# Kernel optimization log

Measured on AMD Instinct MI355X. Metric: run time of the kernel, lower is better.

## Reference

```python
import jax, jax.numpy as jnp
import numpy as np


def setup_inputs() -> dict:
    key = jax.random.key(0)
    kx, kw = jax.random.split(key)
    x = jax.random.normal(kx, (32, 256, 56, 56), dtype=jnp.float32)
    weight = jax.random.uniform(kw, (256, 256, 3, 3), dtype=jnp.float32) * 0.001
    return {"x": x, "weight": weight}


def reference(x, weight):
    # --- binarize activations with straight-through estimator ---
    # forward value = sign(x); gradient flows through clamp(x, -1, 1)
    clipped_x = jnp.clip(x, -1.0, 1.0)
    bx = jax.lax.stop_gradient(jnp.sign(x) - clipped_x) + clipped_x

    # --- binarize weights (per-output-channel mean-centered, scaled sign) ---
    w = weight
    # subtract per-output-channel mean over (in_c, kh, kw)
    bw = w - jnp.mean(w.reshape(w.shape[0], -1), axis=-1)[:, None, None, None]
    # per-output-channel scaling factor = mean |bw| (detached)
    scale = jnp.mean(jnp.abs(bw), axis=(1, 2, 3), keepdims=True)
    scale = jax.lax.stop_gradient(scale)
    clipped_w = jnp.clip(bw, -1.0, 1.0)
    binary_w = jax.lax.stop_gradient(scale * jnp.sign(bw) - clipped_w) + clipped_w

    # --- conv2d, NCHW / OIHW, stride 1, padding 1 ---
    y = jax.lax.conv_general_dilated(
        bx, binary_w,
        window_strides=(1, 1),
        padding=((1, 1), (1, 1)),
        dimension_numbers=("NCHW", "OIHW", "NCHW"),
    )
    return y
```

## Files before the change

kernel.cpp:

```cpp
#include <hip/hip_runtime.h>
#include <cstdint>
#include <cstddef>

#define N_ 32
#define C_ 256
#define H_ 56
#define W_ 56

typedef int v4i __attribute__((ext_vector_type(4)));

static constexpr size_t WB_BYTES = 36ull * 16 * 64 * 16;
static constexpr size_t SC_OFF   = WB_BYTES;

__device__ __forceinline__ uint32_t sgnw(uint32_t u) {
    return (u & 0x7fffffffu) ? (((uint32_t)(((int)u) >> 31) | 1u) & 0xffu) : 0u;
}

__global__ __launch_bounds__(256) void pack_w(const float* __restrict__ wt,
                                              char* __restrict__ wB,
                                              float* __restrict__ scaleg) {
    __shared__ double red[256];
    int o = blockIdx.x, tid = threadIdx.x;
    const float* wo = wt + (size_t)o * 2304;

    double s = 0;
    for (int j = tid; j < 2304; j += 256) s += (double)wo[j];
    red[tid] = s;
    __syncthreads();
    for (int k = 128; k > 0; k >>= 1) {
        if (tid < k) red[tid] += red[tid + k];
        __syncthreads();
    }
    double mean = red[0] / 2304.0;
    __syncthreads();

    double s2 = 0;
    for (int j = tid; j < 2304; j += 256) s2 += fabs((double)wo[j] - mean);
    red[tid] = s2;
    __syncthreads();
    for (int k = 128; k > 0; k >>= 1) {
        if (tid < k) red[tid] += red[tid + k];
        __syncthreads();
    }
    if (tid == 0) scaleg[o] = (float)(red[0] / 2304.0);

    if (tid < 144) {
        int kiter = tid >> 2, q = tid & 3;
        int tap = kiter >> 2, cb = kiter & 3;
        int kh = tap / 3, kw = tap - kh * 3;
        int words[4];
        for (int g = 0; g < 4; ++g) {
            int word = 0;
            for (int b = 0; b < 4; ++b) {
                int c = cb * 64 + q * 16 + g * 4 + b;
                double v = (double)wo[c * 9 + kh * 3 + kw];
                int sg = (v > mean) - (v < mean);
                word |= (sg & 0xff) << (8 * b);
            }
            words[g] = word;
        }
        v4i pk = {words[0], words[1], words[2], words[3]};
        *(v4i*)(wB + (((size_t)kiter * 16 + (o >> 4)) * 64 + q * 16 + (o & 15)) * 16) = pk;
    }
}

__global__ __launch_bounds__(512, 2) void conv_mfma(const float* __restrict__ x,
                                                    const v4i* __restrict__ wB,
                                                    const float* __restrict__ scaleg,
                                                    float* __restrict__ out) {
    __shared__ char xs[6 * 58 * 256];
    int tid = threadIdx.x;
    int wave = tid >> 6, lane = tid & 63;
    int hq = blockIdx.x, n = blockIdx.y;
    int h0 = hq * 4;

    if (tid < 192) {
        int r  = tid >> 5;
        int c2 = tid & 31;
        int wp = (c2 >> 4) * 57;
        int ch = c2 & 15;
        int slot = (ch + wp) & 15;
        v4i z = {0, 0, 0, 0};
        *(v4i*)(xs + ((size_t)(r * 58 + wp) << 8) + (slot << 4)) = z;
    }
    for (int u = tid; u < 6 * 16 * 14; u += 512) {
        int R   = u / 224;
        int rem = u - R * 224;
        int ch  = rem / 14;
        int wq  = rem - ch * 14;
        int ir  = h0 + R - 1;
        if (ir < 0 || ir > 55) {
            v4i z = {0, 0, 0, 0};
#pragma unroll
            for (int h = 0; h < 4; ++h) {
                int wp = 1 + wq * 4 + h;
                int slot = (ch + wp) & 15;
                *(v4i*)(xs + ((size_t)(R * 58 + wp) << 8) + (slot << 4)) = z;
            }
            continue;
        }
        const float* xb = x + ((size_t)n * C_ + ch * 16) * 3136 + ir * 56 + wq * 4;
        uint32_t t[4][4];
#pragma unroll
        for (int p = 0; p < 4; ++p) {
            uint32_t w0, w1, w2, w3;
            {
                float4 v = *(const float4*)(xb + (size_t)(4 * p + 0) * 3136);
                w0 = sgnw(__float_as_uint(v.x)) | (sgnw(__float_as_uint(v.y)) << 8) |
                     (sgnw(__float_as_uint(v.z)) << 16) | (sgnw(__float_as_uint(v.w)) << 24);
            }
            {
                float4 v = *(const float4*)(xb + (size_t)(4 * p + 1) * 3136);
                w1 = sgnw(__float_as_uint(v.x)) | (sgnw(__float_as_uint(v.y)) << 8) |
                     (sgnw(__float_as_uint(v.z)) << 16) | (sgnw(__float_as_uint(v.w)) << 24);
            }
            {
                float4 v = *(const float4*)(xb + (size_t)(4 * p + 2) * 3136);
                w2 = sgnw(__float_as_uint(v.x)) | (sgnw(__float_as_uint(v.y)) << 8) |
                     (sgnw(__float_as_uint(v.z)) << 16) | (sgnw(__float_as_uint(v.w)) << 24);
            }
            {
                float4 v = *(const float4*)(xb + (size_t)(4 * p + 3) * 3136);
                w3 = sgnw(__float_as_uint(v.x)) | (sgnw(__float_as_uint(v.y)) << 8) |
                     (sgnw(__float_as_uint(v.z)) << 16) | (sgnw(__float_as_uint(v.w)) << 24);
            }
            uint32_t lo01 = __builtin_amdgcn_perm(w1, w0, 0x05010400u);
            uint32_t hi01 = __builtin_amdgcn_perm(w1, w0, 0x07030602u);
            uint32_t lo23 = __builtin_amdgcn_perm(w3, w2, 0x05010400u);
            uint32_t hi23 = __builtin_amdgcn_perm(w3, w2, 0x07030602u);
            t[p][0] = __builtin_amdgcn_perm(lo23, lo01, 0x05040100u);
            t[p][1] = __builtin_amdgcn_perm(lo23, lo01, 0x07060302u);
            t[p][2] = __builtin_amdgcn_perm(hi23, hi01, 0x05040100u);
            t[p][3] = __builtin_amdgcn_perm(hi23, hi01, 0x07060302u);
        }
#pragma unroll
        for (int h = 0; h < 4; ++h) {
            int wp = 1 + wq * 4 + h;
            int slot = (ch + wp) & 15;
            v4i c4 = {(int)t[0][h], (int)t[1][h], (int)t[2][h], (int)t[3][h]};
            *(v4i*)(xs + ((size_t)(R * 58 + wp) << 8) + (slot << 4)) = c4;
        }
    }

    int lm = lane & 15, q = lane >> 4;
    int og = wave & 3, mg = wave >> 2;
    int kstart = __builtin_amdgcn_readfirstlane((9 * wave) >> 1);

    int posb[7], slotb[7];
#pragma unroll
    for (int mf = 0; mf < 7; ++mf) {
        int m = mg * 112 + mf * 16 + lm;
        int r = m / 56;
        int wof = m - r * 56;
        posb[mf]  = r * 58 + wof;
        slotb[mf] = q + wof;
    }

    v4i acc[7][4];
#pragma unroll
    for (int mf = 0; mf < 7; ++mf)
#pragma unroll
        for (int of = 0; of < 4; ++of) { v4i z = {0, 0, 0, 0}; acc[mf][of] = z; }

    const v4i* wBw = wB + (size_t)(og * 4) * 64 + lane;

    auto wrap = [&](int t) { int k = kstart + t; return k >= 36 ? k - 36 : k; };
    auto loadB = [&](int k, v4i (&b)[4]) {
#pragma unroll
        for (int of = 0; of < 4; ++of) b[of] = wBw[(size_t)k * 1024 + of * 64];
    };

    __syncthreads();

    v4i bR0[4], bR1[4], bR2[4];
    loadB(wrap(0), bR0);
    loadB(wrap(1), bR1);
    loadB(wrap(2), bR2);

    auto step = [&](v4i (&bReg)[4], int t) {
        int k = wrap(t);
        int tap = k >> 2, cb = k & 3;
        int dh = (tap * 11) >> 5;
        int dw = tap - dh * 3;
        int pofs = dh * 58 + dw;
        int sofs = cb * 4 + dw;
        v4i a[7];
#pragma unroll
        for (int mf = 0; mf < 7; ++mf) {
            int pos  = posb[mf] + pofs;
            int slot = (slotb[mf] + sofs) & 15;
            a[mf] = *(const v4i*)(xs + ((size_t)pos << 8) + ((size_t)slot << 4));
        }
        __builtin_amdgcn_s_setprio(1);
#pragma unroll
        for (int mf = 0; mf < 7; ++mf)
#pragma unroll
            for (int of = 0; of < 4; ++of)
                acc[mf][of] = __builtin_amdgcn_mfma_i32_16x16x64_i8(
                    a[mf], bReg[of], acc[mf][of], 0, 0, 0);
        __builtin_amdgcn_s_setprio(0);
        loadB(wrap(t + 3), bReg);
    };

    for (int t3 = 0; t3 < 12; ++t3) {
        int t = t3 * 3;
        step(bR0, t);
        step(bR1, t + 1);
        step(bR2, t + 2);
    }

#pragma unroll
    for (int of = 0; of < 4; ++of) {
        int o = og * 64 + of * 16 + lm;
        float s = scaleg[o];
#pragma unroll
        for (int mf = 0; mf < 7; ++mf) {
            int m  = mg * 112 + mf * 16 + q * 4;
            int r  = m / 56;
            int wb = m - r * 56;
            float* ob = out + ((size_t)(n * C_ + o) * H_ + h0 + r) * W_ + wb;
            float4 v = {s * (float)acc[mf][of].x, s * (float)acc[mf][of].y,
                        s * (float)acc[mf][of].z, s * (float)acc[mf][of].w};
            *(float4*)ob = v;
        }
    }
}

extern "C" void kernel_launch(void* const* d_in, const int* in_sizes, int n_in,
                              void* d_out, int out_size, void* d_ws, size_t ws_size,
                              hipStream_t stream) {
    const float* x   = (const float*)d_in[0];
    const float* wgt = (const float*)d_in[1];
    float* out = (float*)d_out;
    char* ws = (char*)d_ws;

    char*  wb = ws;
    float* sg = (float*)(ws + SC_OFF);

    pack_w<<<dim3(256), dim3(256), 0, stream>>>(wgt, wb, sg);
    conv_mfma<<<dim3(14, N_), dim3(512), 0, stream>>>(x, (const v4i*)wb, sg, out);
}
```

Before: 246.9 us.

## Overlap halo-row staging with first MFMA steps and swizzle block order

The kernel now stages only the first four input rows into LDS before compute. The last two rows are loaded and packed by half the threads during the first twelve k-steps, which only use taps dh=0,1, and then a barrier precedes the remaining steps. The per-wave k order is reworked so every wave starts within the first 12 k-indices, and block IDs are swizzled to group batches for cache locality. Launch bounds drop to one block per CU, which gives more registers to the prefetch buffers but may reduce latency hiding from occupancy.

```diff
diff --git a/kernel.cpp b/kernel.cpp
--- a/kernel.cpp
+++ b/kernel.cpp
@@ -14,6 +14,10 @@
 
 __device__ __forceinline__ uint32_t sgnw(uint32_t u) {
     return (u & 0x7fffffffu) ? (((uint32_t)(((int)u) >> 31) | 1u) & 0xffu) : 0u;
+}
+__device__ __forceinline__ uint32_t pack4(float4 v) {
+    return sgnw(__float_as_uint(v.x)) | (sgnw(__float_as_uint(v.y)) << 8) |
+           (sgnw(__float_as_uint(v.z)) << 16) | (sgnw(__float_as_uint(v.w)) << 24);
 }
 
 __global__ __launch_bounds__(256) void pack_w(const float* __restrict__ wt,
@@ -64,14 +68,17 @@
     }
 }
 
-__global__ __launch_bounds__(512, 2) void conv_mfma(const float* __restrict__ x,
+__global__ __launch_bounds__(512, 1) void conv_mfma(const float* __restrict__ x,
                                                     const v4i* __restrict__ wB,
                                                     const float* __restrict__ scaleg,
                                                     float* __restrict__ out) {
     __shared__ char xs[6 * 58 * 256];
     int tid = threadIdx.x;
     int wave = tid >> 6, lane = tid & 63;
-    int hq = blockIdx.x, n = blockIdx.y;
+
+    int lin = blockIdx.x + 14 * blockIdx.y;
+    int swz = (lin & 7) * 56 + (lin >> 3);
+    int hq = swz % 14, n = swz / 14;
     int h0 = hq * 4;
 
     if (tid < 192) {
@@ -83,13 +90,13 @@
         v4i z = {0, 0, 0, 0};
         *(v4i*)(xs + ((size_t)(r * 58 + wp) << 8) + (slot << 4)) = z;
     }
-    for (int u = tid; u < 6 * 16 * 14; u += 512) {
+    for (int u = tid; u < 896; u += 512) {
         int R   = u / 224;
         int rem = u - R * 224;
         int ch  = rem / 14;
         int wq  = rem - ch * 14;
         int ir  = h0 + R - 1;
-        if (ir < 0 || ir > 55) {
+        if (ir < 0) {
             v4i z = {0, 0, 0, 0};
 #pragma unroll
             for (int h = 0; h < 4; ++h) {
@@ -100,34 +107,17 @@
             continue;
         }
         const float* xb = x + ((size_t)n * C_ + ch * 16) * 3136 + ir * 56 + wq * 4;
+        uint32_t sw[16];
+#pragma unroll
+        for (int c = 0; c < 16; ++c)
+            sw[c] = pack4(*(const float4*)(xb + (size_t)c * 3136));
         uint32_t t[4][4];
 #pragma unroll
         for (int p = 0; p < 4; ++p) {
-            uint32_t w0, w1, w2, w3;
-            {
-                float4 v = *(const float4*)(xb + (size_t)(4 * p + 0) * 3136);
-                w0 = sgnw(__float_as_uint(v.x)) | (sgnw(__float_as_uint(v.y)) << 8) |
-                     (sgnw(__float_as_uint(v.z)) << 16) | (sgnw(__float_as_uint(v.w)) << 24);
-            }
-            {
-                float4 v = *(const float4*)(xb + (size_t)(4 * p + 1) * 3136);
-                w1 = sgnw(__float_as_uint(v.x)) | (sgnw(__float_as_uint(v.y)) << 8) |
-                     (sgnw(__float_as_uint(v.z)) << 16) | (sgnw(__float_as_uint(v.w)) << 24);
-            }
-            {
-                float4 v = *(const float4*)(xb + (size_t)(4 * p + 2) * 3136);
-                w2 = sgnw(__float_as_uint(v.x)) | (sgnw(__float_as_uint(v.y)) << 8) |
-                     (sgnw(__float_as_uint(v.z)) << 16) | (sgnw(__float_as_uint(v.w)) << 24);
-            }
-            {
-                float4 v = *(const float4*)(xb + (size_t)(4 * p + 3) * 3136);
-                w3 = sgnw(__float_as_uint(v.x)) | (sgnw(__float_as_uint(v.y)) << 8) |
-                     (sgnw(__float_as_uint(v.z)) << 16) | (sgnw(__float_as_uint(v.w)) << 24);
-            }
-            uint32_t lo01 = __builtin_amdgcn_perm(w1, w0, 0x05010400u);
-            uint32_t hi01 = __builtin_amdgcn_perm(w1, w0, 0x07030602u);
-            uint32_t lo23 = __builtin_amdgcn_perm(w3, w2, 0x05010400u);
-            uint32_t hi23 = __builtin_amdgcn_perm(w3, w2, 0x07030602u);
+            uint32_t lo01 = __builtin_amdgcn_perm(sw[4*p+1], sw[4*p+0], 0x05010400u);
+            uint32_t hi01 = __builtin_amdgcn_perm(sw[4*p+1], sw[4*p+0], 0x07030602u);
+            uint32_t lo23 = __builtin_amdgcn_perm(sw[4*p+3], sw[4*p+2], 0x05010400u);
+            uint32_t hi23 = __builtin_amdgcn_perm(sw[4*p+3], sw[4*p+2], 0x07030602u);
             t[p][0] = __builtin_amdgcn_perm(lo23, lo01, 0x05040100u);
             t[p][1] = __builtin_amdgcn_perm(lo23, lo01, 0x07060302u);
             t[p][2] = __builtin_amdgcn_perm(hi23, hi01, 0x05040100u);
@@ -142,9 +132,34 @@
         }
     }
 
+    bool su = (tid < 448);
+    int sR = 0, sch = 0, swq = 0;
+    bool sload = false;
+    const float* sxb = nullptr;
+    if (su) {
+        sR  = 4 + (tid / 224);
+        int rem = tid - (sR - 4) * 224;
+        sch = rem / 14;
+        swq = rem - sch * 14;
+        int sir = h0 + sR - 1;
+        sload = (sir <= 55);
+        if (sload)
+            sxb = x + ((size_t)n * C_ + sch * 16) * 3136 + sir * 56 + swq * 4;
+        else {
+            v4i z = {0, 0, 0, 0};
+#pragma unroll
+            for (int h = 0; h < 4; ++h) {
+                int wp = 1 + swq * 4 + h;
+                int slot = (sch + wp) & 15;
+                *(v4i*)(xs + ((size_t)(sR * 58 + wp) << 8) + (slot << 4)) = z;
+            }
+        }
+    }
+
+    __syncthreads();
+
     int lm = lane & 15, q = lane >> 4;
     int og = wave & 3, mg = wave >> 2;
-    int kstart = __builtin_amdgcn_readfirstlane((9 * wave) >> 1);
 
     int posb[7], slotb[7];
 #pragma unroll
@@ -164,21 +179,28 @@
 
     const v4i* wBw = wB + (size_t)(og * 4) * 64 + lane;
 
-    auto wrap = [&](int t) { int k = kstart + t; return k >= 36 ? k - 36 : k; };
+    auto kof = [&](int t) {
+        if (t >= 36) t -= 36;
+        return (t < 12) ? ((wave + t) % 12) : (12 + (3 * wave + (t - 12)) % 24);
+    };
     auto loadB = [&](int k, v4i (&b)[4]) {
 #pragma unroll
         for (int of = 0; of < 4; ++of) b[of] = wBw[(size_t)k * 1024 + of * 64];
     };
 
-    __syncthreads();
+    float4 fa[8];
+    if (su && sload) {
+#pragma unroll
+        for (int c = 0; c < 8; ++c) fa[c] = *(const float4*)(sxb + (size_t)c * 3136);
+    }
 
     v4i bR0[4], bR1[4], bR2[4];
-    loadB(wrap(0), bR0);
-    loadB(wrap(1), bR1);
-    loadB(wrap(2), bR2);
+    loadB(kof(0), bR0);
+    loadB(kof(1), bR1);
+    loadB(kof(2), bR2);
 
     auto step = [&](v4i (&bReg)[4], int t) {
-        int k = wrap(t);
+        int k = kof(t);
         int tap = k >> 2, cb = k & 3;
         int dh = (tap * 11) >> 5;
         int dw = tap - dh * 3;
@@ -199,14 +221,50 @@
                 acc[mf][of] = __builtin_amdgcn_mfma_i32_16x16x64_i8(
                     a[mf], bReg[of], acc[mf][of], 0, 0, 0);
         __builtin_amdgcn_s_setprio(0);
-        loadB(wrap(t + 3), bReg);
+        loadB(kof(t + 3), bReg);
     };
 
-    for (int t3 = 0; t3 < 12; ++t3) {
-        int t = t3 * 3;
-        step(bR0, t);
-        step(bR1, t + 1);
-        step(bR2, t + 2);
+    uint32_t sw_[16];
+    step(bR0, 0);  step(bR1, 1);  step(bR2, 2);
+    step(bR0, 3);  step(bR1, 4);  step(bR2, 5);
+    if (su && sload) {
+#pragma unroll
+        for (int c = 0; c < 8; ++c) sw_[c] = pack4(fa[c]);
+#pragma unroll
+        for (int c = 0; c < 8; ++c) fa[c] = *(const float4*)(sxb + (size_t)(8 + c) * 3136);
+    }
+    step(bR0, 6);  step(bR1, 7);  step(bR2, 8);
+    step(bR0, 9);  step(bR1, 10); step(bR2, 11);
+    if (su && sload) {
+#pragma unroll
+        for (int c = 0; c < 8; ++c) sw_[8 + c] = pack4(fa[c]);
+        uint32_t t[4][4];
+#pragma unroll
+        for (int p = 0; p < 4; ++p) {
+            uint32_t lo01 = __builtin_amdgcn_perm(sw_[4*p+1], sw_[4*p+0], 0x05010400u);
+            uint32_t hi01 = __builtin_amdgcn_perm(sw_[4*p+1], sw_[4*p+0], 0x07030602u);
+            uint32_t lo23 = __builtin_amdgcn_perm(sw_[4*p+3], sw_[4*p+2], 0x05010400u);
+            uint32_t hi23 = __builtin_amdgcn_perm(sw_[4*p+3], sw_[4*p+2], 0x07030602u);
+            t[p][0] = __builtin_amdgcn_perm(lo23, lo01, 0x05040100u);
+            t[p][1] = __builtin_amdgcn_perm(lo23, lo01, 0x07060302u);
+            t[p][2] = __builtin_amdgcn_perm(hi23, hi01, 0x05040100u);
+            t[p][3] = __builtin_amdgcn_perm(hi23, hi01, 0x07060302u);
+        }
+#pragma unroll
+        for (int h = 0; h < 4; ++h) {
+            int wp = 1 + swq * 4 + h;
+            int slot = (sch + wp) & 15;
+            v4i c4 = {(int)t[0][h], (int)t[1][h], (int)t[2][h], (int)t[3][h]};
+            *(v4i*)(xs + ((size_t)(sR * 58 + wp) << 8) + (slot << 4)) = c4;
+        }
+    }
+    asm volatile("s_waitcnt lgkmcnt(0)" ::: "memory");
+    __builtin_amdgcn_s_barrier();
+    __builtin_amdgcn_sched_barrier(0);
+#pragma unroll 2
+    for (int g = 0; g < 8; ++g) {
+        int t = 12 + 3 * g;
+        step(bR0, t); step(bR1, t + 1); step(bR2, t + 2);
     }
 
 #pragma unroll
```

Measured after the change: 384.4 us. 1.56x slower.

## Shrink conv tile to two output rows with 4 waves and swizzled block order

Applied to the files above, without the earlier changes.

Each block now computes two output rows instead of four, using 256 threads (4 waves, each owning 64 output channels) and a 4-row LDS halo tile. This gives twice as many blocks to spread across CUs and uses less LDS per block. A block-index swizzle interleaves images across consecutive blocks, and the activation sign-packing now issues all 16 channel loads before the byte permutes. In exchange, the halo overhead grows (4 input rows per 2 output rows instead of 6 per 4), and each weight fragment is reused across fewer output rows.

```diff
diff --git a/kernel.cpp b/kernel.cpp
--- a/kernel.cpp
+++ b/kernel.cpp
@@ -14,6 +14,10 @@
 
 __device__ __forceinline__ uint32_t sgnw(uint32_t u) {
     return (u & 0x7fffffffu) ? (((uint32_t)(((int)u) >> 31) | 1u) & 0xffu) : 0u;
+}
+__device__ __forceinline__ uint32_t pack4(float4 v) {
+    return sgnw(__float_as_uint(v.x)) | (sgnw(__float_as_uint(v.y)) << 8) |
+           (sgnw(__float_as_uint(v.z)) << 16) | (sgnw(__float_as_uint(v.w)) << 24);
 }
 
 __global__ __launch_bounds__(256) void pack_w(const float* __restrict__ wt,
@@ -64,17 +68,20 @@
     }
 }
 
-__global__ __launch_bounds__(512, 2) void conv_mfma(const float* __restrict__ x,
+__global__ __launch_bounds__(256, 2) void conv_mfma(const float* __restrict__ x,
                                                     const v4i* __restrict__ wB,
                                                     const float* __restrict__ scaleg,
                                                     float* __restrict__ out) {
-    __shared__ char xs[6 * 58 * 256];
+    __shared__ char xs[4 * 58 * 256];
     int tid = threadIdx.x;
     int wave = tid >> 6, lane = tid & 63;
-    int hq = blockIdx.x, n = blockIdx.y;
-    int h0 = hq * 4;
-
-    if (tid < 192) {
+
+    int lin = blockIdx.x + 28 * blockIdx.y;
+    int swz = (lin & 7) * 112 + (lin >> 3);
+    int hp = swz % 28, n = swz / 28;
+    int h0 = hp * 2;
+
+    if (tid < 128) {
         int r  = tid >> 5;
         int c2 = tid & 31;
         int wp = (c2 >> 4) * 57;
@@ -83,7 +90,7 @@
         v4i z = {0, 0, 0, 0};
         *(v4i*)(xs + ((size_t)(r * 58 + wp) << 8) + (slot << 4)) = z;
     }
-    for (int u = tid; u < 6 * 16 * 14; u += 512) {
+    for (int u = tid; u < 896; u += 256) {
         int R   = u / 224;
         int rem = u - R * 224;
         int ch  = rem / 14;
@@ -100,34 +107,17 @@
             continue;
         }
         const float* xb = x + ((size_t)n * C_ + ch * 16) * 3136 + ir * 56 + wq * 4;
+        uint32_t sw[16];
+#pragma unroll
+        for (int c = 0; c < 16; ++c)
+            sw[c] = pack4(*(const float4*)(xb + (size_t)c * 3136));
         uint32_t t[4][4];
 #pragma unroll
         for (int p = 0; p < 4; ++p) {
-            uint32_t w0, w1, w2, w3;
-            {
-                float4 v = *(const float4*)(xb + (size_t)(4 * p + 0) * 3136);
-                w0 = sgnw(__float_as_uint(v.x)) | (sgnw(__float_as_uint(v.y)) << 8) |
-                     (sgnw(__float_as_uint(v.z)) << 16) | (sgnw(__float_as_uint(v.w)) << 24);
-            }
-            {
-                float4 v = *(const float4*)(xb + (size_t)(4 * p + 1) * 3136);
-                w1 = sgnw(__float_as_uint(v.x)) | (sgnw(__float_as_uint(v.y)) << 8) |
-                     (sgnw(__float_as_uint(v.z)) << 16) | (sgnw(__float_as_uint(v.w)) << 24);
-            }
-            {
-                float4 v = *(const float4*)(xb + (size_t)(4 * p + 2) * 3136);
-                w2 = sgnw(__float_as_uint(v.x)) | (sgnw(__float_as_uint(v.y)) << 8) |
-                     (sgnw(__float_as_uint(v.z)) << 16) | (sgnw(__float_as_uint(v.w)) << 24);
-            }
-            {
-                float4 v = *(const float4*)(xb + (size_t)(4 * p + 3) * 3136);
-                w3 = sgnw(__float_as_uint(v.x)) | (sgnw(__float_as_uint(v.y)) << 8) |
-                     (sgnw(__float_as_uint(v.z)) << 16) | (sgnw(__float_as_uint(v.w)) << 24);
-            }
-            uint32_t lo01 = __builtin_amdgcn_perm(w1, w0, 0x05010400u);
-            uint32_t hi01 = __builtin_amdgcn_perm(w1, w0, 0x07030602u);
-            uint32_t lo23 = __builtin_amdgcn_perm(w3, w2, 0x05010400u);
-            uint32_t hi23 = __builtin_amdgcn_perm(w3, w2, 0x07030602u);
+            uint32_t lo01 = __builtin_amdgcn_perm(sw[4*p+1], sw[4*p+0], 0x05010400u);
+            uint32_t hi01 = __builtin_amdgcn_perm(sw[4*p+1], sw[4*p+0], 0x07030602u);
+            uint32_t lo23 = __builtin_amdgcn_perm(sw[4*p+3], sw[4*p+2], 0x05010400u);
+            uint32_t hi23 = __builtin_amdgcn_perm(sw[4*p+3], sw[4*p+2], 0x07030602u);
             t[p][0] = __builtin_amdgcn_perm(lo23, lo01, 0x05040100u);
             t[p][1] = __builtin_amdgcn_perm(lo23, lo01, 0x07060302u);
             t[p][2] = __builtin_amdgcn_perm(hi23, hi01, 0x05040100u);
@@ -143,13 +133,13 @@
     }
 
     int lm = lane & 15, q = lane >> 4;
-    int og = wave & 3, mg = wave >> 2;
-    int kstart = __builtin_amdgcn_readfirstlane((9 * wave) >> 1);
+    int og = wave;
+    int kstart = __builtin_amdgcn_readfirstlane(wave * 9);
 
     int posb[7], slotb[7];
 #pragma unroll
     for (int mf = 0; mf < 7; ++mf) {
-        int m = mg * 112 + mf * 16 + lm;
+        int m = mf * 16 + lm;
         int r = m / 56;
         int wof = m - r * 56;
         posb[mf]  = r * 58 + wof;
@@ -164,7 +154,12 @@
 
     const v4i* wBw = wB + (size_t)(og * 4) * 64 + lane;
 
-    auto wrap = [&](int t) { int k = kstart + t; return k >= 36 ? k - 36 : k; };
+    auto wrap = [&](int t) {
+        int k = kstart + t;
+        if (k >= 36) k -= 36;
+        if (k >= 36) k -= 36;
+        return k;
+    };
     auto loadB = [&](int k, v4i (&b)[4]) {
 #pragma unroll
         for (int of = 0; of < 4; ++of) b[of] = wBw[(size_t)k * 1024 + of * 64];
@@ -211,11 +206,11 @@
 
 #pragma unroll
     for (int of = 0; of < 4; ++of) {
-        int o = og * 64 + of * 16 + lm;
+        int o = (og * 4 + of) * 16 + lm;
         float s = scaleg[o];
 #pragma unroll
         for (int mf = 0; mf < 7; ++mf) {
-            int m  = mg * 112 + mf * 16 + q * 4;
+            int m  = mf * 16 + q * 4;
             int r  = m / 56;
             int wb = m - r * 56;
             float* ob = out + ((size_t)(n * C_ + o) * H_ + h0 + r) * W_ + wb;
@@ -238,5 +233,5 @@
     float* sg = (float*)(ws + SC_OFF);
 
     pack_w<<<dim3(256), dim3(256), 0, stream>>>(wgt, wb, sg);
-    conv_mfma<<<dim3(14, N_), dim3(512), 0, stream>>>(x, (const v4i*)wb, sg, out);
-}
+    conv_mfma<<<dim3(28, N_), dim3(256), 0, stream>>>(x, (const v4i*)wb, sg, out);
+}
```

Result: no change. 246.1 us (-0.3%).
